# Optimization experiments

Hardware: AMD Instinct MI355X
Metric: run time of the kernel (lower is better)

The kernel has to match this reference:

```python
import jax, jax.numpy as jnp
import numpy as np
from jax import lax

B, T, V, E, H = 8, 512, 32000, 256, 512
NEG = -1e9


def setup_inputs() -> dict:
    key = jax.random.key(0)
    ks = jax.random.split(key, 13)
    g = lambda k, shp, sc: (jax.random.normal(k, shp, jnp.float32) * sc)
    return {
        'x': jax.random.randint(ks[0], (B, T), 0, V),
        'lengths': jax.random.randint(ks[1], (B,), T // 2, T + 1),
        'embed': g(ks[2], (V, E), 0.02),
        'W_ih': g(ks[3], (H, E), 1.0 / np.sqrt(E)),
        'W_hh': g(ks[4], (H, H), 1.0 / np.sqrt(H)),
        'b_ih': g(ks[5], (H,), 0.01),
        'b_hh': g(ks[6], (H,), 0.01),
        'attn_W': g(ks[7], (H, 2 * H), 1.0 / np.sqrt(2 * H)),
        'attn_b': g(ks[8], (H,), 0.01),
        'attn_v': g(ks[9], (1, H), 1.0 / np.sqrt(H)),
        'attn_v_b': g(ks[10], (1,), 0.01),
        'fc_W': g(ks[11], (V, 2 * H), 1.0 / np.sqrt(2 * H)),
        'fc_b': g(ks[12], (V,), 0.01),
    }


def reference(x, lengths, embed, W_ih, W_hh, b_ih, b_hh,
              attn_W, attn_b, attn_v, attn_v_b, fc_W, fc_b):
    b, t = x.shape
    h = W_ih.shape[0]
    # embedding with padding_idx=0 (row 0 forced to zero)
    tab = embed.at[0].set(0.0)
    emb = tab[x]  # [B,T,E]
    # vanilla tanh RNN via scan (precompute input projection)
    xin = emb @ W_ih.T + b_ih  # [B,T,H]

    def rnn_step(hprev, xt):
        hnew = jnp.tanh(xt + hprev @ W_hh.T + b_hh)
        return hnew, hnew

    _, out = lax.scan(rnn_step, jnp.zeros((b, h), xin.dtype), xin.transpose(1, 0, 2))
    out = out.transpose(1, 0, 2)  # [B,T,H]
    # pad_packed_sequence zeros hidden states past each sequence length
    len_mask = jnp.arange(t)[None, :] < lengths[:, None]  # [B,T]
    out = out * len_mask[..., None].astype(out.dtype)

    # additive attention: score(t,s) = v . tanh(W1 h_t + W2 h_s + b)
    W1, W2 = attn_W[:, :h], attn_W[:, h:]
    q = out @ W1.T            # [B,T,H]
    k = out @ W2.T + attn_b   # [B,T,H]
    v = attn_v[0]             # [H]

    def att_row(_, qt):  # qt: [B,H] -> scores over all s: [B,T]
        s = jnp.tanh(qt[:, None, :] + k) @ v + attn_v_b[0]
        return None, s

    _, scores = lax.scan(att_row, None, q.transpose(1, 0, 2))  # [T,B,T]
    scores = scores.transpose(1, 0, 2)  # [B,T(query),T(key)]
    causal = jnp.arange(t)[:, None] >= jnp.arange(t)[None, :]  # s <= t
    valid = causal[None] & len_mask[:, None, :]
    scores = jnp.where(valid, scores, NEG)
    alpha = jax.nn.softmax(scores, axis=-1)
    context = jnp.einsum('bts,bsh->bth', alpha, out)  # [B,T,H]
    feats = jnp.concatenate([out, context], axis=-1)  # [B,T,2H]
    logits = feats @ fc_W.T + fc_b  # [B,T,V]
    return logits
```

## Files before the change

kernel.cpp:

```cpp
#include <hip/hip_runtime.h>
#include <hip/hip_bf16.h>

typedef __attribute__((ext_vector_type(8))) short short8;
typedef __attribute__((ext_vector_type(4))) float f32x4;

#define AL64(p)    __hip_atomic_load((p), __ATOMIC_RELAXED, __HIP_MEMORY_SCOPE_AGENT)
#define AS64(p, v) __hip_atomic_store((p), (v), __ATOMIC_RELAXED, __HIP_MEMORY_SCOPE_AGENT)

__device__ __forceinline__ void glds16(const void* g, void* l) {
  __builtin_amdgcn_global_load_lds(
      (const __attribute__((address_space(1))) unsigned int*)g,
      (__attribute__((address_space(3))) unsigned int*)l, 16, 0, 0);
}

__device__ __forceinline__ void bar_lds() {
  asm volatile("s_waitcnt lgkmcnt(0)\n\ts_barrier" ::: "memory");
}

__device__ __forceinline__ float fast_tanh(float x) {
  float e = __expf(2.0f * x);
  return (e - 1.0f) * __builtin_amdgcn_rcpf(e + 1.0f);
}

__device__ __forceinline__ unsigned short bfh(float f) {
  __hip_bfloat16 h = __float2bfloat16(f);
  return *reinterpret_cast<unsigned short*>(&h);
}
__device__ __forceinline__ float bf2f(unsigned short u) {
  unsigned v = ((unsigned)u) << 16;
  float f;
  __builtin_memcpy(&f, &v, 4);
  return f;
}
__device__ __forceinline__ short bf16r(float f) { return (short)bfh(f); }

union FragU {
  unsigned int u[4];
  short8 s;
};

__global__ __launch_bounds__(256) void k_cvt_bf16(const float* __restrict__ src,
                                                  unsigned short* __restrict__ dst, int n) {
  int i = (blockIdx.x * 256 + threadIdx.x) * 8;
  if (i >= n) return;
  float4 a = *(const float4*)(src + i);
  float4 b = *(const float4*)(src + i + 4);
  short8 v;
  v[0] = bf16r(a.x); v[1] = bf16r(a.y); v[2] = bf16r(a.z); v[3] = bf16r(a.w);
  v[4] = bf16r(b.x); v[5] = bf16r(b.y); v[6] = bf16r(b.z); v[7] = bf16r(b.w);
  *(short8*)(dst + i) = v;
}

__global__ __launch_bounds__(256) void k_xin(const int* __restrict__ x, const float* __restrict__ embed,
                                             const float* __restrict__ W_ih, const float* __restrict__ b_ih,
                                             float* __restrict__ xin) {
  __shared__ float At[64][128];
  __shared__ float Bt[128][64];
  const int tid = threadIdx.x;
  const int bt0 = blockIdx.x * 64, j0 = blockIdx.y * 64;
  const int ty = tid >> 4, tx = tid & 15;
  const int lane = tid & 63, cgrp = tid >> 6;
  float acc[4][4] = {};
  for (int kc = 0; kc < 256; kc += 128) {
#pragma unroll
    for (int rr = 0; rr < 8; ++rr) {
      int row = rr * 8 + (tid >> 5);
      int col = (tid & 31) * 4;
      int tok = x[bt0 + row];
      float4 v = make_float4(0.f, 0.f, 0.f, 0.f);
      if (tok != 0) v = *(const float4*)&embed[(size_t)tok * 256 + kc + col];
      *(float4*)&At[row][col] = v;
    }
#pragma unroll
    for (int cc = 0; cc < 8; ++cc) {
      int col = cgrp * 32 + cc * 4;
      float4 v = *(const float4*)&W_ih[(size_t)(j0 + lane) * 256 + kc + col];
      Bt[col + 0][lane] = v.x; Bt[col + 1][lane] = v.y;
      Bt[col + 2][lane] = v.z; Bt[col + 3][lane] = v.w;
    }
    __syncthreads();
    for (int kk = 0; kk < 128; ++kk) {
      float bv[4];
#pragma unroll
      for (int c = 0; c < 4; ++c) bv[c] = Bt[kk][tx * 4 + c];
#pragma unroll
      for (int a = 0; a < 4; ++a) {
        float av = At[ty * 4 + a][kk];
#pragma unroll
        for (int c = 0; c < 4; ++c) acc[a][c] = fmaf(av, bv[c], acc[a][c]);
      }
    }
    __syncthreads();
  }
#pragma unroll
  for (int a = 0; a < 4; ++a) {
    int m = bt0 + ty * 4 + a;
#pragma unroll
    for (int c = 0; c < 4; ++c) {
      int j = j0 + tx * 4 + c;
      xin[(size_t)m * 512 + j] = acc[a][c] + b_ih[j];
    }
  }
}

__global__ __launch_bounds__(512) void k_rnn(const float* __restrict__ xin, const float* __restrict__ W_hh,
                                             const float* __restrict__ b_hh, const int* __restrict__ lengths,
                                             unsigned long long* mbox, float* __restrict__ out) {
  const int blk = blockIdx.x, tid = threadIdx.x;
  const int w = tid >> 6, l = tid & 63;
  const int jt = w & 3, kh = w >> 2;
  const int j16 = blk * 64 + jt * 16;
  const int r = l & 15;
  const int g = l >> 4;
  const int n = l & 15;

  __shared__ unsigned long long stg[2048];
  __shared__ f32x4 Cbuf[4][64];
  __shared__ float hLf[8][64];
  __shared__ unsigned int hL32[8][64];
  __shared__ int nflag[2];

  short8 bhi[8], blo[8];
  {
    const float* wrow = &W_hh[(size_t)(j16 + n) * 512];
#pragma unroll
    for (int c8 = 0; c8 < 8; ++c8) {
      int c = kh * 8 + c8;
      const float* wp = wrow + c * 32 + g * 8;
      float4 wa = *(const float4*)wp;
      float4 wb = *(const float4*)(wp + 4);
      float wv[8] = {wa.x, wa.y, wa.z, wa.w, wb.x, wb.y, wb.z, wb.w};
#pragma unroll
      for (int e = 0; e < 8; ++e) {
        unsigned short h = bfh(wv[e]);
        bhi[c8][e] = (short)h;
        blo[c8][e] = (short)bfh(wv[e] - bf2f(h));
      }
    }
  }

  float bj = 0.f, xv[4];
  if (w < 4 && l < 32) {
    bj = b_hh[j16 + n];
#pragma unroll
    for (int i = 0; i < 4; ++i)
      xv[i] = xin[((size_t)(g * 4 + i) * 512 + 0) * 512 + j16 + n];
  }
  const int mylen = lengths[tid >> 6 & 7];

  if (tid < 2) nflag[tid] = 0;
  __syncthreads();

  const unsigned long long SENT = ~0ull;

  for (int t = 0; t < 512; ++t) {
    {
      unsigned long long* src = mbox + ((size_t)blk * 16 + (t & 15)) * 2048 + tid * 4;
      const int idx0 = tid * 4;
      const unsigned swz = ((idx0 >> 8) & 7) << 1;
      bool mine = false;
      int round = 0;
      while (true) {
        if (!mine) {
          unsigned long long v0 = AL64(src + 0), v1 = AL64(src + 1);
          unsigned long long v2 = AL64(src + 2), v3 = AL64(src + 3);
          if ((unsigned)v0 != 0xFFFFFFFFu && (unsigned)v1 != 0xFFFFFFFFu &&
              (unsigned)v2 != 0xFFFFFFFFu && (unsigned)v3 != 0xFFFFFFFFu) {
            mine = true;
            stg[(idx0 + 0) ^ swz] = v0; stg[(idx0 + 1) ^ swz] = v1;
            stg[(idx0 + 2) ^ swz] = v2; stg[(idx0 + 3) ^ swz] = v3;
            AS64(src + 0, SENT); AS64(src + 1, SENT);
            AS64(src + 2, SENT); AS64(src + 3, SENT);
          }
        }
        int p = round & 1;
        if (!mine) nflag[p] = 1;
        bar_lds();
        int bad = nflag[p];
        if (tid == 0) nflag[p ^ 1] = 0;
        bar_lds();
        if (!bad) break;
        if (++round == 4096) break;
      }
    }

    f32x4 acc0 = {}, acc1 = {};
#pragma unroll
    for (int c8 = 0; c8 < 8; ++c8) {
      FragU ah, al;
      if (r < 8) {
        int i0 = r * 256 + kh * 128 + c8 * 16 + g * 4;
        unsigned sw = ((i0 >> 8) & 7) << 1;
        unsigned long long u0 = stg[(i0 + 0) ^ sw], u1 = stg[(i0 + 1) ^ sw];
        unsigned long long u2 = stg[(i0 + 2) ^ sw], u3 = stg[(i0 + 3) ^ sw];
        ah.u[0] = (unsigned)u0; al.u[0] = (unsigned)(u0 >> 32);
        ah.u[1] = (unsigned)u1; al.u[1] = (unsigned)(u1 >> 32);
        ah.u[2] = (unsigned)u2; al.u[2] = (unsigned)(u2 >> 32);
        ah.u[3] = (unsigned)u3; al.u[3] = (unsigned)(u3 >> 32);
      } else {
        ah.u[0] = ah.u[1] = ah.u[2] = ah.u[3] = 0u;
        al.u[0] = al.u[1] = al.u[2] = al.u[3] = 0u;
      }
      if (c8 & 1) {
        acc1 = __builtin_amdgcn_mfma_f32_16x16x32_bf16(ah.s, bhi[c8], acc1, 0, 0, 0);
        acc1 = __builtin_amdgcn_mfma_f32_16x16x32_bf16(ah.s, blo[c8], acc1, 0, 0, 0);
        acc1 = __builtin_amdgcn_mfma_f32_16x16x32_bf16(al.s, bhi[c8], acc1, 0, 0, 0);
      } else {
        acc0 = __builtin_amdgcn_mfma_f32_16x16x32_bf16(ah.s, bhi[c8], acc0, 0, 0, 0);
        acc0 = __builtin_amdgcn_mfma_f32_16x16x32_bf16(ah.s, blo[c8], acc0, 0, 0, 0);
        acc0 = __builtin_amdgcn_mfma_f32_16x16x32_bf16(al.s, bhi[c8], acc0, 0, 0, 0);
      }
    }
    f32x4 tot = acc0 + acc1;

    if (w >= 4) Cbuf[w - 4][l] = tot;
    bar_lds();
    if (w < 4) {
      tot += Cbuf[w][l];
      if (l < 32) {
#pragma unroll
        for (int i = 0; i < 4; ++i) {
          int b = g * 4 + i;
          float hn = fast_tanh(xv[i] + tot[i] + bj);
          hLf[b][jt * 16 + n] = hn;
          unsigned hi = bfh(hn);
          unsigned lo = bfh(hn - bf2f((unsigned short)hi));
          hL32[b][jt * 16 + n] = hi | (lo << 16);
        }
        int tt = (t < 511) ? t + 1 : 511;
#pragma unroll
        for (int i = 0; i < 4; ++i)
          xv[i] = xin[((size_t)(g * 4 + i) * 512 + tt) * 512 + j16 + n];
      }
    }
    bar_lds();

    {
      int b = tid >> 6, jl = tid & 63;
      float hv = hLf[b][jl];
      out[((size_t)b * 512 + t) * 512 + blk * 64 + jl] = (t < mylen) ? hv : 0.f;
    }

    if (t < 511) {
      unsigned long long* dst = mbox + ((size_t)w * 16 + ((t + 1) & 15)) * 2048 + blk * 32;
#pragma unroll
      for (int k2 = 0; k2 < 4; ++k2) {
        int idx = l + k2 * 64;
        int b = idx >> 5, jpl = idx & 31;
        unsigned u0 = hL32[b][jpl * 2], u1 = hL32[b][jpl * 2 + 1];
        unsigned hipr = (u0 & 0xffffu) | (u1 << 16);
        unsigned lopr = (u0 >> 16) | (u1 & 0xffff0000u);
        AS64(dst + b * 256 + jpl, (unsigned long long)hipr | ((unsigned long long)lopr << 32));
      }
    }
  }
}

template <int MODE>
__global__ __launch_bounds__(256) void k_qk(const float* __restrict__ out, const float* __restrict__ attn_W,
                                            const float* __restrict__ attn_b, float* __restrict__ dst) {
  __shared__ float At[64][128];
  __shared__ float Bt[128][64];
  const int tid = threadIdx.x;
  const int bt0 = blockIdx.x * 64, j0 = blockIdx.y * 64;
  const int ty = tid >> 4, tx = tid & 15;
  const int lane = tid & 63, cgrp = tid >> 6;
  float acc[4][4] = {};
  for (int kc = 0; kc < 512; kc += 128) {
#pragma unroll
    for (int rr = 0; rr < 8; ++rr) {
      int row = rr * 8 + (tid >> 5);
      int col = (tid & 31) * 4;
      *(float4*)&At[row][col] = *(const float4*)&out[((size_t)bt0 + row) * 512 + kc + col];
    }
#pragma unroll
    for (int cc = 0; cc < 8; ++cc) {
      int col = cgrp * 32 + cc * 4;
      float4 v = *(const float4*)&attn_W[(size_t)(j0 + lane) * 1024 + (MODE ? 512 : 0) + kc + col];
      Bt[col + 0][lane] = v.x; Bt[col + 1][lane] = v.y;
      Bt[col + 2][lane] = v.z; Bt[col + 3][lane] = v.w;
    }
    __syncthreads();
    for (int kk = 0; kk < 128; ++kk) {
      float bv[4];
#pragma unroll
      for (int c = 0; c < 4; ++c) bv[c] = Bt[kk][tx * 4 + c];
#pragma unroll
      for (int a = 0; a < 4; ++a) {
        float av = At[ty * 4 + a][kk];
#pragma unroll
        for (int c = 0; c < 4; ++c) acc[a][c] = fmaf(av, bv[c], acc[a][c]);
      }
    }
    __syncthreads();
  }
#pragma unroll
  for (int a = 0; a < 4; ++a) {
    int bt = bt0 + ty * 4 + a;
#pragma unroll
    for (int c = 0; c < 4; ++c) {
      int j = j0 + tx * 4 + c;
      if (MODE == 0) {
        dst[(size_t)bt * 512 + j] = acc[a][c];
      } else {
        int bb = bt >> 9, tt = bt & 511;
        dst[((size_t)bb * 512 + j) * 512 + tt] = acc[a][c] + attn_b[j];
      }
    }
  }
}

__global__ __launch_bounds__(256) void k_scores(const float* __restrict__ q, const float* __restrict__ kT,
                                                const float* __restrict__ attn_v, const float* __restrict__ attn_v_b,
                                                const int* __restrict__ lengths, float* __restrict__ pbuf) {
  const int b = blockIdx.x, t0 = blockIdx.y * 4;
  const int tid = threadIdx.x;
  __shared__ float qL[4][512];
  __shared__ float vL[512];
  for (int i = tid; i < 4 * 512; i += 256) {
    int rr = i >> 9, h = i & 511;
    qL[rr][h] = q[((size_t)b * 512 + t0 + rr) * 512 + h];
  }
  for (int i = tid; i < 512; i += 256) vL[i] = attn_v[i];
  const float vb = attn_v_b[0];
  const int len = lengths[b];
  __syncthreads();
  const int s_hi = min(t0 + 3, len - 1);
  const float* kTb = kT + (size_t)b * 512 * 512;
#pragma unroll
  for (int si = 0; si < 2; ++si) {
    int s = tid + si * 256;
    float acc[4] = {0.f, 0.f, 0.f, 0.f};
    if (s <= s_hi) {
      for (int h = 0; h < 512; ++h) {
        float kv = kTb[(size_t)h * 512 + s];
        float vh = vL[h];
#pragma unroll
        for (int rr = 0; rr < 4; ++rr) acc[rr] = fmaf(vh, fast_tanh(qL[rr][h] + kv), acc[rr]);
      }
    }
#pragma unroll
    for (int rr = 0; rr < 4; ++rr) {
      int t = t0 + rr;
      bool valid = (s <= t) && (s < len);
      pbuf[((size_t)b * 512 + t) * 512 + s] = valid ? __expf(acc[rr] + vb - 20.f) : 0.f;
    }
  }
}

__global__ __launch_bounds__(256) void k_rowinv(const float* __restrict__ pbuf, float* __restrict__ invl) {
  int row = blockIdx.x * 4 + (threadIdx.x >> 6);
  int lane = threadIdx.x & 63;
  const float* pr = pbuf + (size_t)row * 512;
  float s = 0.f;
#pragma unroll
  for (int i = 0; i < 8; ++i) s += pr[lane + i * 64];
#pragma unroll
  for (int m = 1; m < 64; m <<= 1) s += __shfl_xor(s, m);
  if (lane == 0) invl[row] = 1.0f / s;
}

__global__ __launch_bounds__(256) void k_cvt_out_feats(const float* __restrict__ out,
                                                       unsigned short* __restrict__ feats) {
  int i = (blockIdx.x * 256 + threadIdx.x) * 8;
  int m = i >> 9, c = i & 511;
  float4 a = *(const float4*)(out + i);
  float4 b = *(const float4*)(out + i + 4);
  short8 v;
  v[0] = bf16r(a.x); v[1] = bf16r(a.y); v[2] = bf16r(a.z); v[3] = bf16r(a.w);
  v[4] = bf16r(b.x); v[5] = bf16r(b.y); v[6] = bf16r(b.z); v[7] = bf16r(b.w);
  *(short8*)(feats + (size_t)m * 1024 + c) = v;
}

__global__ __launch_bounds__(256) void k_context(const float* __restrict__ pbuf, const float* __restrict__ out,
                                                 const float* __restrict__ invl, unsigned short* __restrict__ feats) {
  __shared__ float Pt[64][128];
  __shared__ float Ot[128][64];
  const int b = blockIdx.z, t0 = blockIdx.y * 64, h0 = blockIdx.x * 64;
  const int tid = threadIdx.x, ty = tid >> 4, tx = tid & 15;
  float acc[4][4] = {};
  for (int sc = 0; sc < 512; sc += 128) {
#pragma unroll
    for (int rr = 0; rr < 8; ++rr) {
      int row = rr * 8 + (tid >> 5);
      int col = (tid & 31) * 4;
      *(float4*)&Pt[row][col] = *(const float4*)&pbuf[((size_t)b * 512 + t0 + row) * 512 + sc + col];
    }
#pragma unroll
    for (int rr = 0; rr < 8; ++rr) {
      int srow = rr * 16 + (tid >> 4);
      int col = (tid & 15) * 4;
      *(float4*)&Ot[srow][col] = *(const float4*)&out[((size_t)b * 512 + sc + srow) * 512 + h0 + col];
    }
    __syncthreads();
    for (int kk = 0; kk < 128; ++kk) {
      float ov[4];
#pragma unroll
      for (int c = 0; c < 4; ++c) ov[c] = Ot[kk][tx * 4 + c];
#pragma unroll
      for (int a = 0; a < 4; ++a) {
        float pv = Pt[ty * 4 + a][kk];
#pragma unroll
        for (int c = 0; c < 4; ++c) acc[a][c] = fmaf(pv, ov[c], acc[a][c]);
      }
    }
    __syncthreads();
  }
#pragma unroll
  for (int a = 0; a < 4; ++a) {
    int t = t0 + ty * 4 + a;
    float il = invl[b * 512 + t];
#pragma unroll
    for (int c = 0; c < 4; ++c) {
      int h = h0 + tx * 4 + c;
      feats[((size_t)b * 512 + t) * 1024 + 512 + h] = (unsigned short)bf16r(acc[a][c] * il);
    }
  }
}

__global__ __launch_bounds__(256) void k_logits(const unsigned short* __restrict__ A,
                                                const unsigned short* __restrict__ Bw,
                                                const float* __restrict__ bias, float* __restrict__ C) {
  __shared__ unsigned short As[128 * 64];
  __shared__ unsigned short Bs[128 * 64];
  const int tid = threadIdx.x;
  const int wave = tid >> 6, lane = tid & 63;
  const int m0 = blockIdx.x * 128, n0 = blockIdx.y * 128;
  const int wm = (wave >> 1) * 64, wn = (wave & 1) * 64;
  const int lo16 = lane & 15, oct = lane >> 4;
  f32x4 acc[4][4] = {};
  for (int kt = 0; kt < 1024; kt += 64) {
#pragma unroll
    for (int i = 0; i < 4; ++i) {
      int ci = wave * 4 + i;
      int mrow = ci * 8 + (lane >> 3);
      int k8 = (lane & 7) * 8;
      glds16(&A[(size_t)(m0 + mrow) * 1024 + kt + k8], &As[ci * 512]);
      glds16(&Bw[(size_t)(n0 + mrow) * 1024 + kt + k8], &Bs[ci * 512]);
    }
    __syncthreads();
#pragma unroll
    for (int kk = 0; kk < 2; ++kk) {
      short8 af[4], bf[4];
#pragma unroll
      for (int i = 0; i < 4; ++i)
        af[i] = *(const short8*)&As[(wm + i * 16 + lo16) * 64 + kk * 32 + oct * 8];
#pragma unroll
      for (int jn = 0; jn < 4; ++jn)
        bf[jn] = *(const short8*)&Bs[(wn + jn * 16 + lo16) * 64 + kk * 32 + oct * 8];
#pragma unroll
      for (int i = 0; i < 4; ++i)
#pragma unroll
        for (int jn = 0; jn < 4; ++jn)
          acc[i][jn] = __builtin_amdgcn_mfma_f32_16x16x32_bf16(af[i], bf[jn], acc[i][jn], 0, 0, 0);
    }
    __syncthreads();
  }
#pragma unroll
  for (int jn = 0; jn < 4; ++jn) {
    int nn = n0 + wn + jn * 16 + lo16;
    float bv = bias[nn];
#pragma unroll
    for (int i = 0; i < 4; ++i) {
      int mbase = m0 + wm + i * 16 + oct * 4;
#pragma unroll
      for (int rr = 0; rr < 4; ++rr)
        C[(size_t)(mbase + rr) * 32000 + nn] = acc[i][jn][rr] + bv;
    }
  }
}

extern "C" void kernel_launch(void* const* d_in, const int* in_sizes, int n_in,
                              void* d_out, int out_size, void* d_ws, size_t ws_size,
                              hipStream_t stream) {
  const int* x = (const int*)d_in[0];
  const int* lengths = (const int*)d_in[1];
  const float* embed = (const float*)d_in[2];
  const float* W_ih = (const float*)d_in[3];
  const float* W_hh = (const float*)d_in[4];
  const float* b_ih = (const float*)d_in[5];
  const float* b_hh = (const float*)d_in[6];
  const float* attn_W = (const float*)d_in[7];
  const float* attn_b = (const float*)d_in[8];
  const float* attn_v = (const float*)d_in[9];
  const float* attn_v_b = (const float*)d_in[10];
  const float* fc_W = (const float*)d_in[11];
  const float* fc_b = (const float*)d_in[12];
  float* logits = (float*)d_out;

  char* ws = (char*)d_ws;
  const size_t MB8 = 8388608;
  float* xin  = (float*)(ws);
  float* outp = (float*)(ws + 1 * MB8);
  float* q    = (float*)(ws + 2 * MB8);
  float* kT   = (float*)(ws + 3 * MB8);
  float* pbuf = (float*)(ws + 4 * MB8);
  float* invl = (float*)(ws + 5 * MB8);
  unsigned short* feats = (unsigned short*)(ws + 5 * MB8 + 16384);
  unsigned short* fcWb  = (unsigned short*)(ws + 6 * MB8 + 16384);
  unsigned long long* mbox = (unsigned long long*)pbuf;

  hipMemsetAsync(mbox, 0xFF, 8 * 16 * 16384, stream);
  for (int d = 0; d < 8; ++d)
    hipMemsetAsync((char*)mbox + (size_t)d * 16 * 16384, 0x00, 16384, stream);
  k_cvt_bf16<<<16000, 256, 0, stream>>>(fc_W, fcWb, 32768000);
  k_xin<<<dim3(64, 8), 256, 0, stream>>>(x, embed, W_ih, b_ih, xin);
  k_rnn<<<8, 512, 0, stream>>>(xin, W_hh, b_hh, lengths, mbox, outp);
  k_qk<0><<<dim3(64, 8), 256, 0, stream>>>(outp, attn_W, attn_b, q);
  k_qk<1><<<dim3(64, 8), 256, 0, stream>>>(outp, attn_W, attn_b, kT);
  k_scores<<<dim3(8, 128), 256, 0, stream>>>(q, kT, attn_v, attn_v_b, lengths, pbuf);
  k_rowinv<<<1024, 256, 0, stream>>>(pbuf, invl);
  k_cvt_out_feats<<<1024, 256, 0, stream>>>(outp, feats);
  k_context<<<dim3(8, 8, 8), 256, 0, stream>>>(pbuf, outp, invl, feats);
  k_logits<<<dim3(32, 250), 256, 0, stream>>>(feats, fcWb, fc_b, logits);
}
```

Baseline: 2.759 ms.

## Overlap fc_W conversion with RNN, fuse row sums and feats writes, remap logits grid

The fc_W bf16 conversion now runs on extra blocks launched alongside the 8 persistent RNN blocks, so it overlaps the latency-bound recurrence. The RNN step drops one barrier by having both k-halves reduce partial sums symmetrically, and writes mailbox data and output/feats directly from registers using a shuffle. k_scores computes softmax row sums in-kernel, which removes k_rowinv, and the feats conversion is folded into the RNN, which removes k_cvt_out_feats. k_logits uses a 1D grid mapped so that blocks on the same XCD share A rows, aiming for better L2 reuse. The co-resident converter blocks could compete with the RNN blocks for memory bandwidth or delay them.

After: 3.157 ms. +14.4%, slower.

```diff
diff --git a/kernel.cpp b/kernel.cpp
--- a/kernel.cpp
+++ b/kernel.cpp
@@ -38,18 +38,6 @@
   unsigned int u[4];
   short8 s;
 };
-
-__global__ __launch_bounds__(256) void k_cvt_bf16(const float* __restrict__ src,
-                                                  unsigned short* __restrict__ dst, int n) {
-  int i = (blockIdx.x * 256 + threadIdx.x) * 8;
-  if (i >= n) return;
-  float4 a = *(const float4*)(src + i);
-  float4 b = *(const float4*)(src + i + 4);
-  short8 v;
-  v[0] = bf16r(a.x); v[1] = bf16r(a.y); v[2] = bf16r(a.z); v[3] = bf16r(a.w);
-  v[4] = bf16r(b.x); v[5] = bf16r(b.y); v[6] = bf16r(b.z); v[7] = bf16r(b.w);
-  *(short8*)(dst + i) = v;
-}
 
 __global__ __launch_bounds__(256) void k_xin(const int* __restrict__ x, const float* __restrict__ embed,
                                              const float* __restrict__ W_ih, const float* __restrict__ b_ih,
@@ -105,8 +93,23 @@
 
 __global__ __launch_bounds__(512) void k_rnn(const float* __restrict__ xin, const float* __restrict__ W_hh,
                                              const float* __restrict__ b_hh, const int* __restrict__ lengths,
-                                             unsigned long long* mbox, float* __restrict__ out) {
-  const int blk = blockIdx.x, tid = threadIdx.x;
+                                             unsigned long long* mbox, float* __restrict__ out,
+                                             unsigned short* __restrict__ feats,
+                                             const float* __restrict__ fcW, unsigned short* __restrict__ fcWb) {
+  const int tid = threadIdx.x;
+  if (blockIdx.x >= 8) {
+    const size_t stride = (size_t)(gridDim.x - 8) * 512 * 8;
+    for (size_t i = ((size_t)(blockIdx.x - 8) * 512 + tid) * 8; i < 32768000ull; i += stride) {
+      float4 a = *(const float4*)(fcW + i);
+      float4 b = *(const float4*)(fcW + i + 4);
+      short8 v;
+      v[0] = bf16r(a.x); v[1] = bf16r(a.y); v[2] = bf16r(a.z); v[3] = bf16r(a.w);
+      v[4] = bf16r(b.x); v[5] = bf16r(b.y); v[6] = bf16r(b.z); v[7] = bf16r(b.w);
+      *(short8*)(fcWb + i) = v;
+    }
+    return;
+  }
+  const int blk = blockIdx.x;
   const int w = tid >> 6, l = tid & 63;
   const int jt = w & 3, kh = w >> 2;
   const int j16 = blk * 64 + jt * 16;
@@ -115,9 +118,7 @@
   const int n = l & 15;
 
   __shared__ unsigned long long stg[2048];
-  __shared__ f32x4 Cbuf[4][64];
-  __shared__ float hLf[8][64];
-  __shared__ unsigned int hL32[8][64];
+  __shared__ f32x4 Cbuf[2][4][64];
   __shared__ int nflag[2];
 
   short8 bhi[8], blo[8];
@@ -140,24 +141,26 @@
   }
 
   float bj = 0.f, xv[4];
-  if (w < 4 && l < 32) {
+  int len4[4];
+  if (l < 32) {
     bj = b_hh[j16 + n];
 #pragma unroll
-    for (int i = 0; i < 4; ++i)
-      xv[i] = xin[((size_t)(g * 4 + i) * 512 + 0) * 512 + j16 + n];
-  }
-  const int mylen = lengths[tid >> 6 & 7];
+    for (int i = 0; i < 4; ++i) {
+      int b = g * 4 + i;
+      len4[i] = lengths[b];
+      xv[i] = xin[((size_t)b * 512 + 0) * 512 + j16 + n];
+    }
+  }
 
   if (tid < 2) nflag[tid] = 0;
   __syncthreads();
 
   const unsigned long long SENT = ~0ull;
+  const int sgran = tid ^ ((tid >> 6) & 3);
 
   for (int t = 0; t < 512; ++t) {
     {
       unsigned long long* src = mbox + ((size_t)blk * 16 + (t & 15)) * 2048 + tid * 4;
-      const int idx0 = tid * 4;
-      const unsigned swz = ((idx0 >> 8) & 7) << 1;
       bool mine = false;
       int round = 0;
       while (true) {
@@ -167,8 +170,8 @@
           if ((unsigned)v0 != 0xFFFFFFFFu && (unsigned)v1 != 0xFFFFFFFFu &&
               (unsigned)v2 != 0xFFFFFFFFu && (unsigned)v3 != 0xFFFFFFFFu) {
             mine = true;
-            stg[(idx0 + 0) ^ swz] = v0; stg[(idx0 + 1) ^ swz] = v1;
-            stg[(idx0 + 2) ^ swz] = v2; stg[(idx0 + 3) ^ swz] = v3;
+            stg[sgran * 4 + 0] = v0; stg[sgran * 4 + 1] = v1;
+            stg[sgran * 4 + 2] = v2; stg[sgran * 4 + 3] = v3;
             AS64(src + 0, SENT); AS64(src + 1, SENT);
             AS64(src + 2, SENT); AS64(src + 3, SENT);
           }
@@ -180,7 +183,7 @@
         if (tid == 0) nflag[p ^ 1] = 0;
         bar_lds();
         if (!bad) break;
-        if (++round == 4096) break;
+        if (++round == (1 << 16)) break;
       }
     }
 
@@ -189,10 +192,10 @@
     for (int c8 = 0; c8 < 8; ++c8) {
       FragU ah, al;
       if (r < 8) {
-        int i0 = r * 256 + kh * 128 + c8 * 16 + g * 4;
-        unsigned sw = ((i0 >> 8) & 7) << 1;
-        unsigned long long u0 = stg[(i0 + 0) ^ sw], u1 = stg[(i0 + 1) ^ sw];
-        unsigned long long u2 = stg[(i0 + 2) ^ sw], u3 = stg[(i0 + 3) ^ sw];
+        int gran = r * 64 + kh * 32 + c8 * 4 + g;
+        int gs = (gran ^ (r & 3)) * 4;
+        unsigned long long u0 = stg[gs + 0], u1 = stg[gs + 1];
+        unsigned long long u2 = stg[gs + 2], u3 = stg[gs + 3];
         ah.u[0] = (unsigned)u0; al.u[0] = (unsigned)(u0 >> 32);
         ah.u[1] = (unsigned)u1; al.u[1] = (unsigned)(u1 >> 32);
         ah.u[2] = (unsigned)u2; al.u[2] = (unsigned)(u2 >> 32);
@@ -213,44 +216,53 @@
     }
     f32x4 tot = acc0 + acc1;
 
-    if (w >= 4) Cbuf[w - 4][l] = tot;
+    Cbuf[kh][jt][l] = tot;
     bar_lds();
-    if (w < 4) {
-      tot += Cbuf[w][l];
-      if (l < 32) {
+    tot += Cbuf[kh ^ 1][jt][l];
+
+    if (l < 32) {
+      float hn4[4];
+      unsigned pk[4];
+#pragma unroll
+      for (int i = 0; i < 4; ++i) {
+        float hn = fast_tanh(xv[i] + tot[i] + bj);
+        hn4[i] = hn;
+        unsigned hi = bfh(hn);
+        unsigned lo = bfh(hn - bf2f((unsigned short)hi));
+        pk[i] = hi | (lo << 16);
+      }
+      int tt = (t < 511) ? t + 1 : 511;
+#pragma unroll
+      for (int i = 0; i < 4; ++i)
+        xv[i] = xin[((size_t)(g * 4 + i) * 512 + tt) * 512 + j16 + n];
+
+      if (t < 511) {
+        unsigned other[4];
+#pragma unroll
+        for (int i = 0; i < 4; ++i) other[i] = __shfl_xor(pk[i], 1);
+        if ((n & 1) == 0) {
+          const int jp = jt * 8 + (n >> 1);
+#pragma unroll
+          for (int i = 0; i < 4; ++i) {
+            unsigned hipr = (pk[i] & 0xffffu) | ((other[i] & 0xffffu) << 16);
+            unsigned lopr = (pk[i] >> 16) | (other[i] & 0xffff0000u);
+            unsigned long long val = (unsigned long long)hipr | ((unsigned long long)lopr << 32);
+            size_t base = ((size_t)((t + 1) & 15)) * 2048 + (size_t)(g * 4 + i) * 256 + blk * 32 + jp;
+#pragma unroll
+            for (int m4 = 0; m4 < 4; ++m4)
+              AS64(mbox + ((size_t)(kh * 4 + m4) * 16) * 2048 + base, val);
+          }
+        }
+      }
+
+      if (kh == 0) {
 #pragma unroll
         for (int i = 0; i < 4; ++i) {
           int b = g * 4 + i;
-          float hn = fast_tanh(xv[i] + tot[i] + bj);
-          hLf[b][jt * 16 + n] = hn;
-          unsigned hi = bfh(hn);
-          unsigned lo = bfh(hn - bf2f((unsigned short)hi));
-          hL32[b][jt * 16 + n] = hi | (lo << 16);
+          float hv = (t < len4[i]) ? hn4[i] : 0.f;
+          out[((size_t)b * 512 + t) * 512 + j16 + n] = hv;
+          feats[((size_t)b * 512 + t) * 1024 + j16 + n] = bfh(hv);
         }
-        int tt = (t < 511) ? t + 1 : 511;
-#pragma unroll
-        for (int i = 0; i < 4; ++i)
-          xv[i] = xin[((size_t)(g * 4 + i) * 512 + tt) * 512 + j16 + n];
-      }
-    }
-    bar_lds();
-
-    {
-      int b = tid >> 6, jl = tid & 63;
-      float hv = hLf[b][jl];
-      out[((size_t)b * 512 + t) * 512 + blk * 64 + jl] = (t < mylen) ? hv : 0.f;
-    }
-
-    if (t < 511) {
-      unsigned long long* dst = mbox + ((size_t)w * 16 + ((t + 1) & 15)) * 2048 + blk * 32;
-#pragma unroll
-      for (int k2 = 0; k2 < 4; ++k2) {
-        int idx = l + k2 * 64;
-        int b = idx >> 5, jpl = idx & 31;
-        unsigned u0 = hL32[b][jpl * 2], u1 = hL32[b][jpl * 2 + 1];
-        unsigned hipr = (u0 & 0xffffu) | (u1 << 16);
-        unsigned lopr = (u0 >> 16) | (u1 & 0xffff0000u);
-        AS64(dst + b * 256 + jpl, (unsigned long long)hipr | ((unsigned long long)lopr << 32));
       }
     }
   }
@@ -312,11 +324,13 @@
 
 __global__ __launch_bounds__(256) void k_scores(const float* __restrict__ q, const float* __restrict__ kT,
                                                 const float* __restrict__ attn_v, const float* __restrict__ attn_v_b,
-                                                const int* __restrict__ lengths, float* __restrict__ pbuf) {
+                                                const int* __restrict__ lengths, float* __restrict__ pbuf,
+                                                float* __restrict__ invl) {
   const int b = blockIdx.x, t0 = blockIdx.y * 4;
   const int tid = threadIdx.x;
   __shared__ float qL[4][512];
   __shared__ float vL[512];
+  __shared__ float red[4][4];
   for (int i = tid; i < 4 * 512; i += 256) {
     int rr = i >> 9, h = i & 511;
     qL[rr][h] = q[((size_t)b * 512 + t0 + rr) * 512 + h];
@@ -327,6 +341,7 @@
   __syncthreads();
   const int s_hi = min(t0 + 3, len - 1);
   const float* kTb = kT + (size_t)b * 512 * 512;
+  float psum[4] = {0.f, 0.f, 0.f, 0.f};
 #pragma unroll
   for (int si = 0; si < 2; ++si) {
     int s = tid + si * 256;
@@ -343,33 +358,24 @@
     for (int rr = 0; rr < 4; ++rr) {
       int t = t0 + rr;
       bool valid = (s <= t) && (s < len);
-      pbuf[((size_t)b * 512 + t) * 512 + s] = valid ? __expf(acc[rr] + vb - 20.f) : 0.f;
-    }
-  }
-}
-
-__global__ __launch_bounds__(256) void k_rowinv(const float* __restrict__ pbuf, float* __restrict__ invl) {
-  int row = blockIdx.x * 4 + (threadIdx.x >> 6);
-  int lane = threadIdx.x & 63;
-  const float* pr = pbuf + (size_t)row * 512;
-  float s = 0.f;
-#pragma unroll
-  for (int i = 0; i < 8; ++i) s += pr[lane + i * 64];
-#pragma unroll
-  for (int m = 1; m < 64; m <<= 1) s += __shfl_xor(s, m);
-  if (lane == 0) invl[row] = 1.0f / s;
-}
-
-__global__ __launch_bounds__(256) void k_cvt_out_feats(const float* __restrict__ out,
-                                                       unsigned short* __restrict__ feats) {
-  int i = (blockIdx.x * 256 + threadIdx.x) * 8;
-  int m = i >> 9, c = i & 511;
-  float4 a = *(const float4*)(out + i);
-  float4 b = *(const float4*)(out + i + 4);
-  short8 v;
-  v[0] = bf16r(a.x); v[1] = bf16r(a.y); v[2] = bf16r(a.z); v[3] = bf16r(a.w);
-  v[4] = bf16r(b.x); v[5] = bf16r(b.y); v[6] = bf16r(b.z); v[7] = bf16r(b.w);
-  *(short8*)(feats + (size_t)m * 1024 + c) = v;
+      float p = valid ? __expf(acc[rr] + vb - 20.f) : 0.f;
+      pbuf[((size_t)b * 512 + t) * 512 + s] = p;
+      psum[rr] += p;
+    }
+  }
+  const int wv = tid >> 6, ln = tid & 63;
+#pragma unroll
+  for (int rr = 0; rr < 4; ++rr) {
+    float v = psum[rr];
+#pragma unroll
+    for (int m = 1; m < 64; m <<= 1) v += __shfl_xor(v, m);
+    if (ln == 0) red[wv][rr] = v;
+  }
+  __syncthreads();
+  if (tid < 4) {
+    float s = red[0][tid] + red[1][tid] + red[2][tid] + red[3][tid];
+    invl[(size_t)b * 512 + t0 + tid] = 1.0f / s;
+  }
 }
 
 __global__ __launch_bounds__(256) void k_context(const float* __restrict__ pbuf, const float* __restrict__ out,
@@ -421,11 +427,14 @@
 __global__ __launch_bounds__(256) void k_logits(const unsigned short* __restrict__ A,
                                                 const unsigned short* __restrict__ Bw,
                                                 const float* __restrict__ bias, float* __restrict__ C) {
+  const int linb = blockIdx.x;
+  const int xcd = linb & 7, pos = linb >> 3;
+  const int m0 = (xcd * 4 + (pos & 3)) * 128;
+  const int n0 = (pos >> 2) * 128;
   __shared__ unsigned short As[128 * 64];
   __shared__ unsigned short Bs[128 * 64];
   const int tid = threadIdx.x;
   const int wave = tid >> 6, lane = tid & 63;
-  const int m0 = blockIdx.x * 128, n0 = blockIdx.y * 128;
   const int wm = (wave >> 1) * 64, wn = (wave & 1) * 64;
   const int lo16 = lane & 15, oct = lane >> 4;
   f32x4 acc[4][4] = {};
@@ -503,14 +512,11 @@
   hipMemsetAsync(mbox, 0xFF, 8 * 16 * 16384, stream);
   for (int d = 0; d < 8; ++d)
     hipMemsetAsync((char*)mbox + (size_t)d * 16 * 16384, 0x00, 16384, stream);
-  k_cvt_bf16<<<16000, 256, 0, stream>>>(fc_W, fcWb, 32768000);
   k_xin<<<dim3(64, 8), 256, 0, stream>>>(x, embed, W_ih, b_ih, xin);
-  k_rnn<<<8, 512, 0, stream>>>(xin, W_hh, b_hh, lengths, mbox, outp);
+  k_rnn<<<136, 512, 0, stream>>>(xin, W_hh, b_hh, lengths, mbox, outp, feats, fc_W, fcWb);
   k_qk<0><<<dim3(64, 8), 256, 0, stream>>>(outp, attn_W, attn_b, q);
   k_qk<1><<<dim3(64, 8), 256, 0, stream>>>(outp, attn_W, attn_b, kT);
-  k_scores<<<dim3(8, 128), 256, 0, stream>>>(q, kT, attn_v, attn_v_b, lengths, pbuf);
-  k_rowinv<<<1024, 256, 0, stream>>>(pbuf, invl);
-  k_cvt_out_feats<<<1024, 256, 0, stream>>>(outp, feats);
+  k_scores<<<dim3(8, 128), 256, 0, stream>>>(q, kT, attn_v, attn_v_b, lengths, pbuf, invl);
   k_context<<<dim3(8, 8, 8), 256, 0, stream>>>(pbuf, outp, invl, feats);
-  k_logits<<<dim3(32, 250), 256, 0, stream>>>(feats, fcWb, fc_b, logits);
-}
+  k_logits<<<8000, 256, 0, stream>>>(feats, fcWb, fc_b, logits);
+}
```
